# Performance work log

Measured on AMD Instinct MI355X. Metric: run time of the kernel, lower is better.

Reference implementation:

```python
import jax, jax.numpy as jnp
import numpy as np

LAYERS, BLOCKS = 10, 3
NL = LAYERS * BLOCKS
DC, RC, SC, CLASSES, K = 128, 128, 256, 256, 2
SR = 4096  # number of output samples sliced from the end
N, L, EN = 4, 8192, 16


def _conv1x1(x, w):
    # x: [N, Cin, L], w: [Cout, Cin] -> [N, Cout, L]
    return jnp.einsum('ncl,oc->nol', x, w)


def _condition(x, enc):
    # x: [N, C, L], enc: [N, C, En], L % En == 0; tiled periodic add (faithful to the view trick)
    n, c, l = x.shape
    en = enc.shape[2]
    return (x.reshape(n, c, l // en, en) + enc[:, :, None, :]).reshape(n, c, l)


def _dilated_causal_conv(x, w, d):
    # kernel_size=2 causal dilated conv. x: [N, Cin, L], w: [Cout, Cin, 2]
    xs = jnp.pad(x, ((0, 0), (0, 0), (d, 0)))[:, :, :x.shape[2]]  # x delayed by d
    return jnp.einsum('ncl,oc->nol', xs, w[:, :, 0]) + jnp.einsum('ncl,oc->nol', x, w[:, :, 1])


def setup_inputs() -> dict:
    key = jax.random.key(0)
    ks = jax.random.split(key, 12)
    s = 0.05
    return {
        'x': jax.random.normal(ks[0], (N, CLASSES, L), jnp.float32),
        'en': jax.random.normal(ks[1], (N, CLASSES, EN), jnp.float32),
        'start1_w': jax.random.normal(ks[2], (RC, CLASSES), jnp.float32) * s,
        'start2_w': jax.random.normal(ks[3], (SC, RC), jnp.float32) * s,
        'cond_w': jax.random.normal(ks[4], (NL, 2 * DC, CLASSES), jnp.float32) * s,
        'dil_w': jax.random.normal(ks[5], (NL, 2 * DC, RC, K), jnp.float32) * s,
        'res_w': jax.random.normal(ks[6], (NL, RC, DC), jnp.float32) * s,
        'skip_w': jax.random.normal(ks[7], (NL, SC, DC), jnp.float32) * s,
        'end1_w': jax.random.normal(ks[8], (CLASSES, SC), jnp.float32) * s,
        'end1_b': jnp.zeros((CLASSES,), jnp.float32),
        'end2_w': jax.random.normal(ks[9], (CLASSES, CLASSES), jnp.float32) * s,
        'end2_b': jnp.zeros((CLASSES,), jnp.float32),
    }


def reference(x, en, start1_w, start2_w, cond_w, dil_w, res_w, skip_w,
              end1_w, end1_b, end2_w, end2_b):
    l = _conv1x1(x, start1_w)          # [N, RC, L]
    s = _conv1x1(l, start2_w)          # [N, SC, L]
    for i in range(NL):
        dil = 2 ** (i % LAYERS)
        d = _dilated_causal_conv(l, dil_w[i], dil)      # [N, 2*DC, L]
        d = _condition(d, _conv1x1(en, cond_w[i]))
        g = jax.nn.sigmoid(d[:, :DC]) * jnp.tanh(d[:, DC:])  # gated, [N, DC, L]
        l = l + _conv1x1(g, res_w[i])
        s = s + _conv1x1(g, skip_w[i])
    s = jax.nn.relu(s)
    s = _conv1x1(s, end1_w) + end1_b[None, :, None]
    s = _condition(s, _conv1x1(en, end2_w) + end2_b[None, :, None])
    s = jax.nn.relu(s)
    return s[:, :, -SR:]
```

## Files before the change

### kernel.cpp

```cpp
#include <hip/hip_runtime.h>

typedef __bf16 bf16_t;
typedef __bf16 bf16x8 __attribute__((ext_vector_type(8)));
typedef __bf16 bf16x4 __attribute__((ext_vector_type(4)));
typedef float  f32x4  __attribute__((ext_vector_type(4)));
typedef int    i32x4  __attribute__((ext_vector_type(4)));

#define PL 136
#define PX 264

__device__ __forceinline__ f32x4 mfma16(bf16x8 a, bf16x8 b, f32x4 c) {
    return __builtin_amdgcn_mfma_f32_16x16x32_bf16(a, b, c, 0, 0, 0);
}

__device__ __forceinline__ void barrier_nodrain() {
    asm volatile("s_waitcnt lgkmcnt(0)" ::: "memory");
    __builtin_amdgcn_sched_barrier(0);
    __builtin_amdgcn_s_barrier();
    __builtin_amdgcn_sched_barrier(0);
}

__device__ __forceinline__ void conv8(const float* __restrict__ src,
                                      bf16_t* __restrict__ dst,
                                      int g, int M, int K) {
    int MK8 = (M * K) >> 3;
    int lay = g / MK8;
    int r = g - lay * MK8;
    int lane = r & 63, rest = r >> 6;
    int KB = K >> 5;
    int kb = rest % KB, mt = rest / KB;
    int m = mt * 16 + (lane & 15);
    int k = kb * 32 + ((lane >> 4) << 3);
    const float* s = src + (size_t)lay * M * K + (size_t)m * K + k;
    f32x4 v0 = *(const f32x4*)s;
    f32x4 v1 = *(const f32x4*)(s + 4);
    bf16x8 o;
    o[0] = (bf16_t)v0[0]; o[1] = (bf16_t)v0[1]; o[2] = (bf16_t)v0[2]; o[3] = (bf16_t)v0[3];
    o[4] = (bf16_t)v1[0]; o[5] = (bf16_t)v1[1]; o[6] = (bf16_t)v1[2]; o[7] = (bf16_t)v1[3];
    *(bf16x8*)(dst + (size_t)g * 8) = o;
}

__global__ __launch_bounds__(256) void k_prep(
                       const float* __restrict__ rw, const float* __restrict__ kw,
                       const float* __restrict__ s1w, const float* __restrict__ s2w,
                       const float* __restrict__ e1w, const float* __restrict__ dwt,
                       const float* __restrict__ cond_w, const float* __restrict__ end2_w,
                       const float* __restrict__ end2_b, const float* __restrict__ en,
                       bf16_t* __restrict__ Ares, bf16_t* __restrict__ Askp,
                       bf16_t* __restrict__ A1, bf16_t* __restrict__ A2,
                       bf16_t* __restrict__ Ae, bf16_t* __restrict__ Adil,
                       float* __restrict__ cond_all, float* __restrict__ cond2) {
    if (blockIdx.x >= 1744) {
        __shared__ f32x4 en_s[1024];
        __shared__ f32x4 red[1024];
        int bi = blockIdx.x - 1744;
        int i = bi >> 4;
        int n = (bi >> 2) & 3;
        int og = bi & 3;
        int tid = threadIdx.x;
        const f32x4* ep = (const f32x4*)(en + (size_t)n * 4096);
        for (int idx = tid; idx < 1024; idx += 256) en_s[idx] = ep[idx];
        __syncthreads();
        int o_loc = tid >> 2, part = tid & 3;
        int o = og * 64 + o_loc;
        const float* W = (i < 30) ? cond_w + ((size_t)i * 256 + o) * 256
                                  : end2_w + (size_t)o * 256;
        const float* Wp = W + part * 64;
        f32x4 a0 = {0.f,0.f,0.f,0.f}, a1 = a0, a2 = a0, a3 = a0;
        for (int c = 0; c < 64; c += 4) {
            f32x4 wv = *(const f32x4*)(Wp + c);
            int cg2 = part * 64 + c;
            #pragma unroll
            for (int cc = 0; cc < 4; ++cc) {
                float wf = wv[cc];
                a0 += wf * en_s[(cg2 + cc) * 4 + 0];
                a1 += wf * en_s[(cg2 + cc) * 4 + 1];
                a2 += wf * en_s[(cg2 + cc) * 4 + 2];
                a3 += wf * en_s[(cg2 + cc) * 4 + 3];
            }
        }
        red[tid * 4 + 0] = a0; red[tid * 4 + 1] = a1;
        red[tid * 4 + 2] = a2; red[tid * 4 + 3] = a3;
        __syncthreads();
        if (tid < 64) {
            int o2 = og * 64 + tid;
            float bias = (i < 30) ? 0.f : end2_b[o2];
            float* dst = (i < 30) ? cond_all + (((size_t)i * 4 + n) * 256 + o2) * 16
                                  : cond2 + ((size_t)n * 256 + o2) * 16;
            f32x4* d4 = (f32x4*)dst;
            #pragma unroll
            for (int t = 0; t < 4; ++t) {
                f32x4 s = red[(tid * 4 + 0) * 4 + t] + red[(tid * 4 + 1) * 4 + t]
                        + red[(tid * 4 + 2) * 4 + t] + red[(tid * 4 + 3) * 4 + t];
                d4[t] = s + bias;
            }
        }
        return;
    }
    int g = blockIdx.x * 256 + threadIdx.x;
    if (g < 61440) { conv8(rw, Ares, g, 128, 128); return; }
    g -= 61440;
    if (g < 122880) { conv8(kw, Askp, g, 256, 128); return; }
    g -= 122880;
    if (g < 4096) { conv8(s1w, A1, g, 128, 256); return; }
    g -= 4096;
    if (g < 4096) { conv8(s2w, A2, g, 256, 128); return; }
    g -= 4096;
    if (g < 8192) { conv8(e1w, Ae, g, 256, 256); return; }
    g -= 8192;
    {
        int lay = g >> 13, r = g & 8191;
        int lane = r & 63, rest = r >> 6;
        int kb = rest & 7, mt = rest >> 3;
        int m = mt * 16 + (lane & 15);
        int k0 = kb * 32 + ((lane >> 4) << 3);
        int sel = (k0 < 128) ? 0 : 1;
        int kk = (k0 < 128) ? k0 : k0 - 128;
        const float* s = dwt + (((size_t)lay * 256 + m) * 128 + kk) * 2;
        f32x4 c0 = *(const f32x4*)(s);
        f32x4 c1 = *(const f32x4*)(s + 4);
        f32x4 c2 = *(const f32x4*)(s + 8);
        f32x4 c3 = *(const f32x4*)(s + 12);
        bf16x8 o;
        o[0] = (bf16_t)c0[sel];     o[1] = (bf16_t)c0[2 + sel];
        o[2] = (bf16_t)c1[sel];     o[3] = (bf16_t)c1[2 + sel];
        o[4] = (bf16_t)c2[sel];     o[5] = (bf16_t)c2[2 + sel];
        o[6] = (bf16_t)c3[sel];     o[7] = (bf16_t)c3[2 + sel];
        *(bf16x8*)(Adil + (size_t)lay * 65536 + (size_t)r * 8) = o;
    }
}

__global__ __launch_bounds__(512, 4) void k_start(
    const float* __restrict__ x, bf16_t* __restrict__ la, float* __restrict__ sbuf,
    const bf16_t* __restrict__ A1, const bf16_t* __restrict__ A2, int t_base)
{
    __shared__ __align__(16) bf16_t xt[64 * PX];
    __shared__ __align__(16) bf16_t l0[64 * PL];
    int tid = threadIdx.x;
    int n = blockIdx.y, t0 = t_base + blockIdx.x * 64;
    int lane = tid & 63, w = tid >> 6, i16 = lane & 15, q = lane >> 4;
    f32x4 z = {0.f,0.f,0.f,0.f};
    {
        int t = tid & 63;
        for (int c = tid >> 6; c < 256; c += 8)
            xt[t * PX + c] = (bf16_t)x[((size_t)n * 256 + c) * 8192 + t0 + t];
    }
    __syncthreads();
    f32x4 acc[4] = {z,z,z,z};
    #pragma unroll
    for (int kb = 0; kb < 8; ++kb) {
        int koff = kb * 32 + q * 8;
        bf16x8 bf[4];
        #pragma unroll
        for (int nt = 0; nt < 4; ++nt)
            bf[nt] = *(const bf16x8*)(xt + (nt * 16 + i16) * PX + koff);
        bf16x8 af = *(const bf16x8*)(A1 + (((size_t)w * 8 + kb) * 64 + lane) * 8);
        #pragma unroll
        for (int nt = 0; nt < 4; ++nt) acc[nt] = mfma16(af, bf[nt], acc[nt]);
    }
    #pragma unroll
    for (int nt = 0; nt < 4; ++nt)
        #pragma unroll
        for (int j = 0; j < 4; ++j)
            l0[(nt * 16 + i16) * PL + w * 16 + q * 4 + j] = (bf16_t)acc[nt][j];
    __syncthreads();
    {
        int r = tid >> 4, col = (tid & 15) * 8;
        #pragma unroll
        for (int p = 0; p < 2; ++p) {
            int rr = r + p * 32;
            *(i32x4*)(la + ((size_t)n * 8192 + t0 + rr) * 128 + col) =
                *(const i32x4*)(l0 + rr * PL + col);
        }
    }
    if (t0 >= 4096) {
        f32x4 a2[2][4] = {{z,z,z,z},{z,z,z,z}};
        #pragma unroll
        for (int kb = 0; kb < 4; ++kb) {
            int koff = kb * 32 + q * 8;
            bf16x8 bf[4];
            #pragma unroll
            for (int nt = 0; nt < 4; ++nt)
                bf[nt] = *(const bf16x8*)(l0 + (nt * 16 + i16) * PL + koff);
            #pragma unroll
            for (int mt2 = 0; mt2 < 2; ++mt2) {
                bf16x8 af = *(const bf16x8*)(A2 + ((((size_t)2 * w + mt2) * 4 + kb) * 64 + lane) * 8);
                #pragma unroll
                for (int nt = 0; nt < 4; ++nt) a2[mt2][nt] = mfma16(af, bf[nt], a2[mt2][nt]);
            }
        }
        float* sp = sbuf + (size_t)n * 256 * 4096 + (t0 - 4096);
        #pragma unroll
        for (int mt2 = 0; mt2 < 2; ++mt2)
            #pragma unroll
            for (int nt = 0; nt < 4; ++nt)
                #pragma unroll
                for (int j = 0; j < 4; ++j) {
                    int o = (2 * w + mt2) * 16 + q * 4 + j;
                    sp[(size_t)o * 4096 + nt * 16 + i16] = a2[mt2][nt][j];
                }
    }
}

template<int USEG>
__global__ __launch_bounds__(512, 2) void k_fuse(
    const bf16_t* __restrict__ l_in, bf16_t* __restrict__ l_out,
    bf16_t* __restrict__ G,
    const bf16_t* __restrict__ Adil, const bf16_t* __restrict__ Ares,
    const float* __restrict__ condA, int aG, int g0)
{
    __shared__ __align__(16) bf16_t bufA[192 * PL];
    __shared__ __align__(16) bf16_t bufB[192 * PL];
    __shared__ __align__(16) bf16_t sm2[32 * PL];
    int tid = threadIdx.x;
    int n = blockIdx.y, t0 = aG + blockIdx.x * 128;
    int lane = tid & 63, w = tid >> 6, i16 = lane & 15, q = lane >> 4;
    f32x4 z = {0.f,0.f,0.f,0.f};
    int c_base = w * 16 + q * 4;
    size_t base = (size_t)n * 8192;
    {
        int rr0 = tid >> 4, col = (tid & 15) * 8;
        for (int rr = rr0; rr < 192; rr += 32) {
            int t = t0 - 64 + rr;
            i32x4 v = {0, 0, 0, 0};
            if (t >= 0) v = *(const i32x4*)(l_in + (base + t) * 128 + col);
            *(i32x4*)(bufA + rr * PL + col) = v;
        }
    }
    bf16_t* bin = bufA;
    bf16_t* bout = bufB;
    barrier_nodrain();
    #pragma unroll 1
    for (int k = 0; k < 6; ++k) {
        int i = g0 + k;
        int d = 1 << k;
        const bf16x8* AdF = (const bf16x8*)(Adil + (size_t)i * 65536);
        const bf16x8* ArF = (const bf16x8*)(Ares + (size_t)i * 16384);
        const float* cond = condA + ((size_t)i * 4 + n) * 4096;
        bf16_t* Gl = G + (size_t)i * (4ull * 4096 * 128);
        float cv_s[4], cv_t[4];
        #pragma unroll
        for (int j = 0; j < 4; ++j) {
            cv_s[j] = cond[(c_base + j) * 16 + i16];
            cv_t[j] = cond[(c_base + j + 128) * 16 + i16];
        }
        bf16x8 a_s[8], a_t[8];
        #pragma unroll
        for (int kb = 0; kb < 8; ++kb) {
            a_s[kb] = AdF[((size_t)w * 8 + kb) * 64 + lane];
            a_t[kb] = AdF[((size_t)(w + 8) * 8 + kb) * 64 + lane];
        }
        bf16x8 ar[4];
        #pragma unroll
        for (int kb = 0; kb < 4; ++kb)
            ar[kb] = ArF[((size_t)w * 4 + kb) * 64 + lane];
        #pragma unroll 1
        for (int r0 = 0; r0 < 192; r0 += 32) {
            f32x4 accs[2] = {z,z}, acct[2] = {z,z};
            #pragma unroll
            for (int kb = 0; kb < 8; ++kb) {
                int koff = (kb & 3) * 32 + q * 8;
                bf16x8 bf[2];
                #pragma unroll
                for (int nt = 0; nt < 2; ++nt) {
                    int rr = r0 + nt * 16 + i16;
                    int dr = (kb < 4) ? (rr - d) : rr;
                    if (dr < 0) dr = 0;
                    bf[nt] = *(const bf16x8*)(bin + dr * PL + koff);
                }
                #pragma unroll
                for (int nt = 0; nt < 2; ++nt) {
                    accs[nt] = mfma16(a_s[kb], bf[nt], accs[nt]);
                    acct[nt] = mfma16(a_t[kb], bf[nt], acct[nt]);
                }
            }
            #pragma unroll
            for (int nt = 0; nt < 2; ++nt) {
                bf16x4 g4;
                #pragma unroll
                for (int j = 0; j < 4; ++j) {
                    float vlo = accs[nt][j] + cv_s[j];
                    float vhi = acct[nt][j] + cv_t[j];
                    float sg = 1.0f / (1.0f + __expf(-vlo));
                    float th = 1.0f - 2.0f / (1.0f + __expf(2.0f * vhi));
                    g4[j] = (bf16_t)(sg * th);
                }
                *(bf16x4*)(sm2 + (nt * 16 + i16) * PL + c_base) = g4;
            }
            barrier_nodrain();
            int t_chunk = t0 + (r0 - 64);
            if (USEG && r0 >= 64 && t_chunk >= 4096) {
                int tt = ((tid & 256) >> 4) + (tid & 15);
                int cc = ((tid >> 6) & 3) * 32 + ((tid >> 4) & 3) * 8;
                bf16x8 gv = *(const bf16x8*)(sm2 + tt * PL + cc);
                *(bf16x8*)(Gl + ((size_t)n * 4096 + (t_chunk - 4096)) * 128 + tid * 8) = gv;
            }
            f32x4 acc2[2] = {z,z};
            #pragma unroll
            for (int kb = 0; kb < 4; ++kb) {
                int koff = kb * 32 + q * 8;
                #pragma unroll
                for (int nt = 0; nt < 2; ++nt) {
                    bf16x8 bf = *(const bf16x8*)(sm2 + (nt * 16 + i16) * PL + koff);
                    acc2[nt] = mfma16(ar[kb], bf, acc2[nt]);
                }
            }
            #pragma unroll
            for (int nt = 0; nt < 2; ++nt) {
                int rr = r0 + nt * 16 + i16;
                bf16x4 lv = *(const bf16x4*)(bin + rr * PL + c_base);
                bf16x4 o4;
                #pragma unroll
                for (int j = 0; j < 4; ++j)
                    o4[j] = (bf16_t)((float)lv[j] + acc2[nt][j]);
                *(bf16x4*)(bout + rr * PL + c_base) = o4;
            }
            barrier_nodrain();
        }
        bf16_t* tsw = bin; bin = bout; bout = tsw;
    }
    {
        int rr0 = tid >> 4, col = (tid & 15) * 8;
        for (int rr = 64 + rr0; rr < 192; rr += 32) {
            *(i32x4*)(l_out + (base + t0 - 64 + rr) * 128 + col) =
                *(const i32x4*)(bin + rr * PL + col);
        }
    }
}

template<int USEG>
__global__ __launch_bounds__(512, 4) void k_layer(
    const bf16_t* __restrict__ l_in, bf16_t* __restrict__ l_out,
    float* __restrict__ sbuf, bf16_t* __restrict__ Gl,
    const bf16_t* __restrict__ Ad, const bf16_t* __restrict__ Ar,
    const bf16_t* __restrict__ Ak, const float* __restrict__ condL,
    int dil, int t_base, int do_res)
{
    __shared__ __align__(16) bf16_t smA[64 * PL];
    __shared__ __align__(16) bf16_t sm2[32 * PL];
    int tid = threadIdx.x;
    int n = blockIdx.y, t0 = t_base + blockIdx.x * 32;
    int lane = tid & 63, w = tid >> 6, i16 = lane & 15, q = lane >> 4;
    f32x4 z = {0.f,0.f,0.f,0.f};
    const float* cond = condL + (size_t)n * 4096;
    int r = tid >> 4, col = (tid & 15) * 8;
    int c_base = w * 16 + q * 4;
    size_t base = (size_t)n * 8192;

    float cv_s[4], cv_t[4];
    #pragma unroll
    for (int j = 0; j < 4; ++j) {
        cv_s[j] = cond[(c_base + j) * 16 + i16];
        cv_t[j] = cond[(c_base + j + 128) * 16 + i16];
    }
    const bf16x8* AdF = (const bf16x8*)Ad;
    bf16x8 a_s[8], a_t[8];
    #pragma unroll
    for (int kb = 0; kb < 8; ++kb) {
        a_s[kb] = AdF[((size_t)w * 8 + kb) * 64 + lane];
        a_t[kb] = AdF[((size_t)(w + 8) * 8 + kb) * 64 + lane];
    }

    const bf16_t* curp;
    const bf16_t* delp;
    if (dil < 32) {
        int cnt = (32 + dil) * 16;
        for (int idx = tid; idx < cnt; idx += 512) {
            int rr = idx >> 4, c2 = (idx & 15) * 8;
            *(i32x4*)(smA + rr * PL + c2) =
                *(const i32x4*)(l_in + (base + t0 - dil + rr) * 128 + c2);
        }
        delp = smA; curp = smA + dil * PL;
    } else {
        *(i32x4*)(smA + r * PL + col) =
            *(const i32x4*)(l_in + (base + t0 + r) * 128 + col);
        int gp = t0 - dil + r;
        i32x4 v = {0, 0, 0, 0};
        if (gp >= 0) v = *(const i32x4*)(l_in + (base + gp) * 128 + col);
        *(i32x4*)(smA + (32 + r) * PL + col) = v;
        curp = smA; delp = smA + 32 * PL;
    }
    barrier_nodrain();

    f32x4 accs[2] = {z,z}, acct[2] = {z,z};
    #pragma unroll
    for (int kb = 0; kb < 8; ++kb) {
        const bf16_t* bsrc = (kb < 4) ? delp : curp;
        int koff = (kb & 3) * 32 + q * 8;
        bf16x8 bf[2];
        #pragma unroll
        for (int nt = 0; nt < 2; ++nt)
            bf[nt] = *(const bf16x8*)(bsrc + (nt * 16 + i16) * PL + koff);
        #pragma unroll
        for (int nt = 0; nt < 2; ++nt) {
            accs[nt] = mfma16(a_s[kb], bf[nt], accs[nt]);
            acct[nt] = mfma16(a_t[kb], bf[nt], acct[nt]);
        }
    }

    const bf16x8* ArF = (const bf16x8*)Ar;
    bf16x8 ar[4];
    if (do_res) {
        #pragma unroll
        for (int kb = 0; kb < 4; ++kb)
            ar[kb] = ArF[((size_t)w * 4 + kb) * 64 + lane];
    }

    {
        #pragma unroll
        for (int nt = 0; nt < 2; ++nt) {
            bf16x4 g4;
            #pragma unroll
            for (int j = 0; j < 4; ++j) {
                float vlo = accs[nt][j] + cv_s[j];
                float vhi = acct[nt][j] + cv_t[j];
                float sg = 1.0f / (1.0f + __expf(-vlo));
                float th = 1.0f - 2.0f / (1.0f + __expf(2.0f * vhi));
                g4[j] = (bf16_t)(sg * th);
            }
            *(bf16x4*)(sm2 + (nt * 16 + i16) * PL + c_base) = g4;
        }
    }
    barrier_nodrain();

    if (USEG) {
        if (t0 >= 4096) {
            int tt = ((tid & 256) >> 4) + (tid & 15);
            int cc = ((tid >> 6) & 3) * 32 + ((tid >> 4) & 3) * 8;
            bf16x8 gv = *(const bf16x8*)(sm2 + tt * PL + cc);
            *(bf16x8*)(Gl + ((size_t)n * 4096 + (t0 - 4096)) * 128 + tid * 8) = gv;
        }
    }

    f32x4 acc2[2] = {z,z};
    if (do_res || !USEG) {
        int do_skip = (!USEG) && (t0 >= 4096);
        f32x4 acc3[2][2] = {{z,z},{z,z}};
        const bf16x8* AkF = (const bf16x8*)Ak;
        #pragma unroll
        for (int kb = 0; kb < 4; ++kb) {
            int koff = kb * 32 + q * 8;
            bf16x8 bf[2];
            #pragma unroll
            for (int nt = 0; nt < 2; ++nt)
                bf[nt] = *(const bf16x8*)(sm2 + (nt * 16 + i16) * PL + koff);
            if (do_res) {
                #pragma unroll
                for (int nt = 0; nt < 2; ++nt) acc2[nt] = mfma16(ar[kb], bf[nt], acc2[nt]);
            }
            if (do_skip) {
                #pragma unroll
                for (int mt2 = 0; mt2 < 2; ++mt2) {
                    bf16x8 ak = AkF[((size_t)(2 * w + mt2) * 4 + kb) * 64 + lane];
                    #pragma unroll
                    for (int nt = 0; nt < 2; ++nt)
                        acc3[mt2][nt] = mfma16(ak, bf[nt], acc3[mt2][nt]);
                }
            }
        }
        if (do_skip) {
            float* sp = sbuf + (size_t)n * 256 * 4096 + (t0 - 4096);
            #pragma unroll
            for (int mt2 = 0; mt2 < 2; ++mt2)
                #pragma unroll
                for (int nt = 0; nt < 2; ++nt)
                    #pragma unroll
                    for (int j = 0; j < 4; ++j) {
                        int o = (2 * w + mt2) * 16 + q * 4 + j;
                        sp[(size_t)o * 4096 + nt * 16 + i16] += acc3[mt2][nt][j];
                    }
        }
    }

    if (do_res) {
        #pragma unroll
        for (int nt = 0; nt < 2; ++nt) {
            int trow = (nt * 16 + i16) * PL;
            bf16x4 lv = *(const bf16x4*)(curp + trow + c_base);
            bf16x4 o4;
            #pragma unroll
            for (int j = 0; j < 4; ++j)
                o4[j] = (bf16_t)((float)lv[j] + acc2[nt][j]);
            *(bf16x4*)(l_out + (base + t0 + nt * 16 + i16) * 128 + c_base) = o4;
        }
    }
}

#define SKIP_HALF(I, AKU, AKP, GW0, GW1)                                        \
    {                                                                           \
        const int i_ = (I);                                                     \
        if (i_ + 1 < 30) {                                                      \
            bf16_t* db = gbuf[(i_ + 1) & 1];                                    \
            *(i32x4*)(db + tid * 8) = GW0;                                      \
            *(i32x4*)(db + 4096 + tid * 8) = GW1;                               \
        }                                                                       \
        if (i_ + 3 < 30) {                                                      \
            const bf16_t* srcp = gb + (size_t)(i_ + 3) * GLS;                   \
            GW0 = *(const i32x4*)(srcp);                                        \
            GW1 = *(const i32x4*)(srcp + 4096);                                 \
        }                                                                       \
        if (i_ + 1 < 30) {                                                      \
            const bf16x8* An = (const bf16x8*)(Askp + (size_t)(i_ + 1) * 32768);\
            _Pragma("unroll")                                                   \
            for (int kb = 0; kb < 4; ++kb) {                                    \
                AKP[2 * kb]     = An[fi0 + kb * 64];                            \
                AKP[2 * kb + 1] = An[fi1 + kb * 64];                            \
            }                                                                   \
        }                                                                       \
        const bf16_t* gp_ = gbuf[i_ & 1];                                       \
        _Pragma("unroll")                                                       \
        for (int kb = 0; kb < 4; ++kb) {                                        \
            _Pragma("unroll")                                                   \
            for (int nt = 0; nt < 4; ++nt) {                                    \
                bf16x8 bfv = *(const bf16x8*)(gp_ + (nt >> 1) * 4096 +          \
                              (((nt & 1) * 4 + kb) * 64 + lane) * 8);           \
                acc[0][nt] = mfma16(AKU[2 * kb], bfv, acc[0][nt]);              \
                acc[1][nt] = mfma16(AKU[2 * kb + 1], bfv, acc[1][nt]);          \
            }                                                                   \
        }                                                                       \
        if (i_ + 1 < 30) {                                                      \
            asm volatile("s_waitcnt lgkmcnt(0)" ::: "memory");                  \
            __builtin_amdgcn_sched_barrier(0);                                  \
            __builtin_amdgcn_s_barrier();                                       \
            __builtin_amdgcn_sched_barrier(0);                                  \
        }                                                                       \
    }

__global__ __launch_bounds__(512, 2) void k_skip(
    const bf16_t* __restrict__ G, float* __restrict__ sbuf,
    const bf16_t* __restrict__ Askp)
{
    __shared__ __align__(16) bf16_t gbuf[2][8192];
    int tid = threadIdx.x;
    int n = blockIdx.y, t0 = blockIdx.x * 64;
    int lane = tid & 63, w = tid >> 6, i16 = lane & 15, q = lane >> 4;
    f32x4 z = {0.f,0.f,0.f,0.f};
    f32x4 acc[2][4] = {{z,z,z,z},{z,z,z,z}};
    const size_t GLS = (size_t)4 * 4096 * 128;
    const bf16_t* gb = G + ((size_t)n * 4096 + t0) * 128 + tid * 8;
    int fi0 = (2 * w) * 256 + lane;
    int fi1 = fi0 + 256;
    bf16x8 akA[8], akB[8];
    {
        const bf16x8* A0 = (const bf16x8*)Askp;
        #pragma unroll
        for (int kb = 0; kb < 4; ++kb) {
            akA[2 * kb]     = A0[fi0 + kb * 64];
            akA[2 * kb + 1] = A0[fi1 + kb * 64];
        }
    }
    i32x4 gA0, gA1, gB0, gB1;
    {
        i32x4 t0v = *(const i32x4*)(gb);
        i32x4 t1v = *(const i32x4*)(gb + 4096);
        *(i32x4*)(gbuf[0] + tid * 8) = t0v;
        *(i32x4*)(gbuf[0] + 4096 + tid * 8) = t1v;
    }
    gA0 = *(const i32x4*)(gb + 1 * GLS);
    gA1 = *(const i32x4*)(gb + 1 * GLS + 4096);
    gB0 = *(const i32x4*)(gb + 2 * GLS);
    gB1 = *(const i32x4*)(gb + 2 * GLS + 4096);
    __syncthreads();
    #pragma unroll 1
    for (int ii = 0; ii < 30; ii += 2) {
        SKIP_HALF(ii,     akA, akB, gA0, gA1)
        SKIP_HALF(ii + 1, akB, akA, gB0, gB1)
    }
    float* sp = sbuf + (size_t)n * 256 * 4096 + t0;
    #pragma unroll
    for (int mt2 = 0; mt2 < 2; ++mt2)
        #pragma unroll
        for (int nt = 0; nt < 4; ++nt)
            #pragma unroll
            for (int j = 0; j < 4; ++j) {
                int o = (2 * w + mt2) * 16 + q * 4 + j;
                sp[(size_t)o * 4096 + nt * 16 + i16] += acc[mt2][nt][j];
            }
}

__global__ __launch_bounds__(512) void k_end(
    const float* __restrict__ sbuf, float* __restrict__ out,
    const bf16_t* __restrict__ Ae, const float* __restrict__ cond2,
    const float* __restrict__ b1)
{
    __shared__ __align__(16) bf16_t st[64 * PX];
    __shared__ float c2[4096];
    __shared__ float b1s[256];
    int tid = threadIdx.x;
    int n = blockIdx.y, t0 = blockIdx.x * 64;
    int lane = tid & 63, w = tid >> 6, i16 = lane & 15, q = lane >> 4;
    f32x4 z = {0.f,0.f,0.f,0.f};
    {
        int t = tid & 63;
        for (int c = tid >> 6; c < 256; c += 8) {
            float v = sbuf[((size_t)n * 256 + c) * 4096 + t0 + t];
            st[t * PX + c] = (bf16_t)fmaxf(v, 0.f);
        }
        const f32x4* cc = (const f32x4*)(cond2 + (size_t)n * 4096);
        for (int idx = tid; idx < 1024; idx += 512) ((f32x4*)c2)[idx] = cc[idx];
        if (tid < 64) ((f32x4*)b1s)[tid] = ((const f32x4*)b1)[tid];
    }
    __syncthreads();
    f32x4 acc[2][4] = {{z,z,z,z},{z,z,z,z}};
    #pragma unroll
    for (int kb = 0; kb < 8; ++kb) {
        int koff = kb * 32 + q * 8;
        bf16x8 bf[4];
        #pragma unroll
        for (int nt = 0; nt < 4; ++nt)
            bf[nt] = *(const bf16x8*)(st + (nt * 16 + i16) * PX + koff);
        #pragma unroll
        for (int mt2 = 0; mt2 < 2; ++mt2) {
            bf16x8 af = *(const bf16x8*)(Ae + ((((size_t)2 * w + mt2) * 8 + kb) * 64 + lane) * 8);
            #pragma unroll
            for (int nt = 0; nt < 4; ++nt) acc[mt2][nt] = mfma16(af, bf[nt], acc[mt2][nt]);
        }
    }
    #pragma unroll
    for (int mt2 = 0; mt2 < 2; ++mt2)
        #pragma unroll
        for (int j = 0; j < 4; ++j) {
            int o = (2 * w + mt2) * 16 + q * 4 + j;
            float bb = b1s[o] + c2[o * 16 + i16];
            #pragma unroll
            for (int nt = 0; nt < 4; ++nt) {
                float v = acc[mt2][nt][j] + bb;
                out[((size_t)n * 256 + o) * 4096 + t0 + nt * 16 + i16] = fmaxf(v, 0.f);
            }
        }
}

extern "C" void kernel_launch(void* const* d_in, const int* in_sizes, int n_in,
                              void* d_out, int out_size, void* d_ws, size_t ws_size,
                              hipStream_t stream) {
    const float* x   = (const float*)d_in[0];
    const float* en  = (const float*)d_in[1];
    const float* s1w = (const float*)d_in[2];
    const float* s2w = (const float*)d_in[3];
    const float* cw  = (const float*)d_in[4];
    const float* dw  = (const float*)d_in[5];
    const float* rw  = (const float*)d_in[6];
    const float* kw  = (const float*)d_in[7];
    const float* e1w = (const float*)d_in[8];
    const float* e1b = (const float*)d_in[9];
    const float* e2w = (const float*)d_in[10];
    const float* e2b = (const float*)d_in[11];
    float* out = (float*)d_out;

    char* p = (char*)d_ws;
    auto take = [&](size_t bytes) {
        char* r = p;
        p += (bytes + 255) & ~(size_t)255;
        return r;
    };
    bf16_t* A1   = (bf16_t*)take((size_t)128 * 256 * 2);
    bf16_t* A2   = (bf16_t*)take((size_t)256 * 128 * 2);
    bf16_t* Ae   = (bf16_t*)take((size_t)256 * 256 * 2);
    bf16_t* Adil = (bf16_t*)take((size_t)30 * 65536 * 2);
    bf16_t* Ares = (bf16_t*)take((size_t)30 * 16384 * 2);
    bf16_t* Askp = (bf16_t*)take((size_t)30 * 32768 * 2);
    float*  condA= (float*)take((size_t)30 * 16384 * 4);
    float*  cond2= (float*)take((size_t)16384 * 4);
    bf16_t* la   = (bf16_t*)take((size_t)4 * 8192 * 128 * 2);
    bf16_t* lb   = (bf16_t*)take((size_t)4 * 8192 * 128 * 2);
    float*  sbuf = (float*)take((size_t)4 * 256 * 4096 * 4);
    bf16_t* G    = (bf16_t*)take((size_t)30 * 4 * 4096 * 128 * 2);
    bool useG = ((size_t)(p - (char*)d_ws) <= ws_size);

    k_prep<<<2240, 256, 0, stream>>>(rw, kw, s1w, s2w, e1w, dw,
                                     cw, e2w, e2b, en,
                                     Ares, Askp, A1, A2, Ae, Adil, condA, cond2);

    int a[30];
    a[29] = 4096;
    for (int i = 28; i >= 0; --i) {
        int nx = a[i + 1] - (1 << ((i + 1) % 10));
        a[i] = nx < 4096 ? (nx & ~63) : 4096;
    }

    k_start<<<dim3(127, 4), 512, 0, stream>>>(x, la, sbuf, A1, A2, 64);

    bf16_t* src = la;
    bf16_t* dst = lb;
    if (useG) {
        for (int g = 0; g < 3; ++g) {
            int g0 = g * 10;
            int aG = a[g0] & ~127;
            dim3 gridF((8192 - aG) / 128, 4);
            k_fuse<1><<<gridF, 512, 0, stream>>>(src, dst, G, Adil, Ares,
                                                 condA, aG, g0);
            { bf16_t* t = src; src = dst; dst = t; }
            for (int i = g0 + 6; i < g0 + 10; ++i) {
                dim3 grid2((8192 - a[i]) / 32, 4);
                k_layer<1><<<grid2, 512, 0, stream>>>(src, dst, sbuf,
                    G + (size_t)i * 4 * 4096 * 128,
                    Adil + (size_t)i * 65536, Ares + (size_t)i * 16384,
                    Askp + (size_t)i * 32768, condA + (size_t)i * 16384,
                    1 << (i % 10), a[i], i < 29 ? 1 : 0);
                bf16_t* t = src; src = dst; dst = t;
            }
        }
        k_skip<<<dim3(64, 4), 512, 0, stream>>>(G, sbuf, Askp);
    } else {
        for (int i = 0; i < 30; ++i) {
            dim3 grid((8192 - a[i]) / 32, 4);
            k_layer<0><<<grid, 512, 0, stream>>>(src, dst, sbuf, (bf16_t*)nullptr,
                Adil + (size_t)i * 65536, Ares + (size_t)i * 16384,
                Askp + (size_t)i * 32768, condA + (size_t)i * 16384,
                1 << (i % 10), a[i], i < 29 ? 1 : 0);
            bf16_t* t = src; src = dst; dst = t;
        }
    }
    k_end<<<dim3(64, 4), 512, 0, stream>>>(sbuf, out, Ae, cond2, e1b);
}
```

Before: 614.1 us.

## Split k_fuse across 1024 threads with double-buffered gate tile and fewer barriers

Doubles the k_fuse block to 1024 threads so each wave handles a single 16-row N-tile instead of two. The gate staging buffer is double-buffered, which removes one of the two block barriers per 32-row chunk. The goal is more latency hiding and less barrier stalling in the fused six-layer kernel. The launch bound of (1024,4) pushes the compiler toward a very small register budget. With about 80 VGPRs of weight fragments held per wave, that risks heavy spilling, and LDS use limits residency anyway.

```diff
diff --git a/kernel.cpp b/kernel.cpp
--- a/kernel.cpp
+++ b/kernel.cpp
@@ -203,7 +203,7 @@
 }
 
 template<int USEG>
-__global__ __launch_bounds__(512, 2) void k_fuse(
+__global__ __launch_bounds__(1024, 4) void k_fuse(
     const bf16_t* __restrict__ l_in, bf16_t* __restrict__ l_out,
     bf16_t* __restrict__ G,
     const bf16_t* __restrict__ Adil, const bf16_t* __restrict__ Ares,
@@ -211,16 +211,18 @@
 {
     __shared__ __align__(16) bf16_t bufA[192 * PL];
     __shared__ __align__(16) bf16_t bufB[192 * PL];
-    __shared__ __align__(16) bf16_t sm2[32 * PL];
+    __shared__ __align__(16) bf16_t sm2[2][32 * PL];
     int tid = threadIdx.x;
     int n = blockIdx.y, t0 = aG + blockIdx.x * 128;
-    int lane = tid & 63, w = tid >> 6, i16 = lane & 15, q = lane >> 4;
+    int lane = tid & 63, w = tid >> 6;
+    int wo = w >> 1, ntf = w & 1;
+    int i16 = lane & 15, q = lane >> 4;
     f32x4 z = {0.f,0.f,0.f,0.f};
-    int c_base = w * 16 + q * 4;
+    int c_base = wo * 16 + q * 4;
     size_t base = (size_t)n * 8192;
     {
         int rr0 = tid >> 4, col = (tid & 15) * 8;
-        for (int rr = rr0; rr < 192; rr += 32) {
+        for (int rr = rr0; rr < 192; rr += 64) {
             int t = t0 - 64 + rr;
             i32x4 v = {0, 0, 0, 0};
             if (t >= 0) v = *(const i32x4*)(l_in + (base + t) * 128 + col);
@@ -230,6 +232,7 @@
     bf16_t* bin = bufA;
     bf16_t* bout = bufB;
     barrier_nodrain();
+    int p = 0;
     #pragma unroll 1
     for (int k = 0; k < 6; ++k) {
         int i = g0 + k;
@@ -247,81 +250,71 @@
         bf16x8 a_s[8], a_t[8];
         #pragma unroll
         for (int kb = 0; kb < 8; ++kb) {
-            a_s[kb] = AdF[((size_t)w * 8 + kb) * 64 + lane];
-            a_t[kb] = AdF[((size_t)(w + 8) * 8 + kb) * 64 + lane];
+            a_s[kb] = AdF[((size_t)wo * 8 + kb) * 64 + lane];
+            a_t[kb] = AdF[((size_t)(wo + 8) * 8 + kb) * 64 + lane];
         }
         bf16x8 ar[4];
         #pragma unroll
         for (int kb = 0; kb < 4; ++kb)
-            ar[kb] = ArF[((size_t)w * 4 + kb) * 64 + lane];
+            ar[kb] = ArF[((size_t)wo * 4 + kb) * 64 + lane];
         #pragma unroll 1
         for (int r0 = 0; r0 < 192; r0 += 32) {
-            f32x4 accs[2] = {z,z}, acct[2] = {z,z};
+            int rr = r0 + ntf * 16 + i16;
+            int dr = rr - d; if (dr < 0) dr = 0;
+            f32x4 accs = z, acct = z;
             #pragma unroll
             for (int kb = 0; kb < 8; ++kb) {
                 int koff = (kb & 3) * 32 + q * 8;
-                bf16x8 bf[2];
-                #pragma unroll
-                for (int nt = 0; nt < 2; ++nt) {
-                    int rr = r0 + nt * 16 + i16;
-                    int dr = (kb < 4) ? (rr - d) : rr;
-                    if (dr < 0) dr = 0;
-                    bf[nt] = *(const bf16x8*)(bin + dr * PL + koff);
-                }
-                #pragma unroll
-                for (int nt = 0; nt < 2; ++nt) {
-                    accs[nt] = mfma16(a_s[kb], bf[nt], accs[nt]);
-                    acct[nt] = mfma16(a_t[kb], bf[nt], acct[nt]);
-                }
-            }
-            #pragma unroll
-            for (int nt = 0; nt < 2; ++nt) {
+                const bf16_t* brow = (kb < 4) ? (bin + dr * PL) : (bin + rr * PL);
+                bf16x8 bf = *(const bf16x8*)(brow + koff);
+                accs = mfma16(a_s[kb], bf, accs);
+                acct = mfma16(a_t[kb], bf, acct);
+            }
+            bf16_t* s2 = sm2[p];
+            {
                 bf16x4 g4;
                 #pragma unroll
                 for (int j = 0; j < 4; ++j) {
-                    float vlo = accs[nt][j] + cv_s[j];
-                    float vhi = acct[nt][j] + cv_t[j];
+                    float vlo = accs[j] + cv_s[j];
+                    float vhi = acct[j] + cv_t[j];
                     float sg = 1.0f / (1.0f + __expf(-vlo));
                     float th = 1.0f - 2.0f / (1.0f + __expf(2.0f * vhi));
                     g4[j] = (bf16_t)(sg * th);
                 }
-                *(bf16x4*)(sm2 + (nt * 16 + i16) * PL + c_base) = g4;
+                *(bf16x4*)(s2 + (ntf * 16 + i16) * PL + c_base) = g4;
             }
             barrier_nodrain();
             int t_chunk = t0 + (r0 - 64);
             if (USEG && r0 >= 64 && t_chunk >= 4096) {
-                int tt = ((tid & 256) >> 4) + (tid & 15);
-                int cc = ((tid >> 6) & 3) * 32 + ((tid >> 4) & 3) * 8;
-                bf16x8 gv = *(const bf16x8*)(sm2 + tt * PL + cc);
-                *(bf16x8*)(Gl + ((size_t)n * 4096 + (t_chunk - 4096)) * 128 + tid * 8) = gv;
-            }
-            f32x4 acc2[2] = {z,z};
+                int u = tid >> 1, half = tid & 1;
+                int tt = ((u & 256) >> 4) + (u & 15);
+                int cc = ((u >> 6) & 3) * 32 + ((u >> 4) & 3) * 8 + half * 4;
+                *(bf16x4*)(Gl + ((size_t)n * 4096 + (t_chunk - 4096)) * 128
+                              + (size_t)tid * 4)
+                    = *(const bf16x4*)(s2 + tt * PL + cc);
+            }
+            f32x4 acc2 = z;
             #pragma unroll
             for (int kb = 0; kb < 4; ++kb) {
-                int koff = kb * 32 + q * 8;
-                #pragma unroll
-                for (int nt = 0; nt < 2; ++nt) {
-                    bf16x8 bf = *(const bf16x8*)(sm2 + (nt * 16 + i16) * PL + koff);
-                    acc2[nt] = mfma16(ar[kb], bf, acc2[nt]);
-                }
-            }
-            #pragma unroll
-            for (int nt = 0; nt < 2; ++nt) {
-                int rr = r0 + nt * 16 + i16;
+                bf16x8 bf = *(const bf16x8*)(s2 + (ntf * 16 + i16) * PL + kb * 32 + q * 8);
+                acc2 = mfma16(ar[kb], bf, acc2);
+            }
+            {
                 bf16x4 lv = *(const bf16x4*)(bin + rr * PL + c_base);
                 bf16x4 o4;
                 #pragma unroll
                 for (int j = 0; j < 4; ++j)
-                    o4[j] = (bf16_t)((float)lv[j] + acc2[nt][j]);
+                    o4[j] = (bf16_t)((float)lv[j] + acc2[j]);
                 *(bf16x4*)(bout + rr * PL + c_base) = o4;
             }
-            barrier_nodrain();
-        }
+            p ^= 1;
+        }
+        barrier_nodrain();
         bf16_t* tsw = bin; bin = bout; bout = tsw;
     }
     {
         int rr0 = tid >> 4, col = (tid & 15) * 8;
-        for (int rr = 64 + rr0; rr < 192; rr += 32) {
+        for (int rr = 64 + rr0; rr < 192; rr += 64) {
             *(i32x4*)(l_out + (base + t0 - 64 + rr) * 128 + col) =
                 *(const i32x4*)(bin + rr * PL + col);
         }
@@ -687,8 +680,8 @@
             int g0 = g * 10;
             int aG = a[g0] & ~127;
             dim3 gridF((8192 - aG) / 128, 4);
-            k_fuse<1><<<gridF, 512, 0, stream>>>(src, dst, G, Adil, Ares,
-                                                 condA, aG, g0);
+            k_fuse<1><<<gridF, 1024, 0, stream>>>(src, dst, G, Adil, Ares,
+                                                  condA, aG, g0);
             { bf16_t* t = src; src = dst; dst = t; }
             for (int i = g0 + 6; i < g0 + 10; ++i) {
                 dim3 grid2((8192 - a[i]) / 32, 4);
```

Result: slower. 628.1 us (+2.3%).
